# Kernel tuning notes

Hardware: AMD Instinct MI355X
Metric: run time of the kernel (lower is better)

## Reference

```python
import jax, jax.numpy as jnp
import numpy as np

EMBED_DIM = 1024
HEAD_SIZE = 256
B, T = 8, 2048


def setup_inputs() -> dict:
    key = jax.random.key(0)
    kx, kq, kk, kv = jax.random.split(key, 4)
    x = jax.random.normal(kx, (B, T, EMBED_DIM), dtype=jnp.float32)
    # torch Linear(E, H, bias=False): weight [H, E], y = x @ W.T; store as [E, H]
    s = 1.0 / np.sqrt(EMBED_DIM)
    Wq = jax.random.uniform(kq, (EMBED_DIM, HEAD_SIZE), jnp.float32, -s, s)
    Wk = jax.random.uniform(kk, (EMBED_DIM, HEAD_SIZE), jnp.float32, -s, s)
    Wv = jax.random.uniform(kv, (EMBED_DIM, HEAD_SIZE), jnp.float32, -s, s)
    return {"x": x, "Wq": Wq, "Wk": Wk, "Wv": Wv}


def reference(x, Wq, Wk, Wv):
    # x: [B, T, E]
    q = jnp.einsum("bte,eh->bth", x, Wq)
    k = jnp.einsum("bte,eh->bth", x, Wk)
    v = jnp.einsum("bte,eh->bth", x, Wv)
    scale = HEAD_SIZE ** -0.5
    scores = jnp.einsum("bth,bsh->bts", q, k) * scale  # [B, T, T]
    t = x.shape[1]
    causal = jnp.tril(jnp.ones((t, t), dtype=bool))
    scores = jnp.where(causal, scores, -jnp.inf)
    attn = jax.nn.softmax(scores, axis=-1)  # dropout p=0.0 -> identity
    return jnp.einsum("bts,bsh->bth", attn, v)
```

## Files before the change

kernel.cpp:

```cpp
#include <hip/hip_runtime.h>
#include <stdint.h>

#define EMBED 1024
#define HEAD  256
#define BATCH 8
#define SEQ   2048
#define NTOK  (BATCH*SEQ)

typedef __attribute__((ext_vector_type(8)))  short  s16x8;
typedef __attribute__((ext_vector_type(4)))  float  f32x4;
typedef __attribute__((ext_vector_type(16))) float  f32x16;
typedef __attribute__((ext_vector_type(4)))  unsigned short u16x4;

__device__ __forceinline__ unsigned short f2bf(float f) {
  union { float f; uint32_t u; } v; v.f = f;
  return (unsigned short)((v.u + 0x7FFFu + ((v.u >> 16) & 1u)) >> 16);
}

__device__ __forceinline__ uint32_t cvtpk(float a, float b) {
  uint32_t r;
  asm("v_cvt_pk_bf16_f32 %0, %1, %2" : "=v"(r) : "v"(a), "v"(b));
  return r;
}

__device__ __forceinline__ void gload_lds16(const void* g, void* l) {
  __builtin_amdgcn_global_load_lds((const __attribute__((address_space(1))) void*)g,
                                   (__attribute__((address_space(3))) void*)l, 16, 0, 0);
}

__global__ __launch_bounds__(256) void wt_kernel(const float* __restrict__ Wq,
                                                 const float* __restrict__ Wk,
                                                 const float* __restrict__ Wv,
                                                 unsigned short* __restrict__ Wt) {
  int idx = blockIdx.x * 256 + threadIdx.x;
  int e  = idx & (EMBED - 1);
  int hw = idx >> 10;
  int w  = hw >> 8;
  int h  = hw & 255;
  const float* W = (w == 0) ? Wq : (w == 1) ? Wk : Wv;
  float sc = (w == 0) ? 0.0625f : 1.0f;
  Wt[idx] = f2bf(W[(size_t)e * HEAD + h] * sc);
}

__global__ __launch_bounds__(256) void xprep_kernel(const float* __restrict__ x,
                                                    unsigned short* __restrict__ xb) {
  size_t i8 = ((size_t)blockIdx.x * 256 + threadIdx.x) * 8;
  f32x4 f0 = *(const f32x4*)(x + i8);
  f32x4 f1 = *(const f32x4*)(x + i8 + 4);
  u16x4 p0, p1;
  #pragma unroll
  for (int j = 0; j < 4; j++) { p0[j] = f2bf(f0[j]); p1[j] = f2bf(f1[j]); }
  *(u16x4*)(xb + i8)     = p0;
  *(u16x4*)(xb + i8 + 4) = p1;
}

__global__ __launch_bounds__(256) void proj_kernel(const unsigned short* __restrict__ xb,
    const unsigned short* __restrict__ Wt,
    unsigned short* __restrict__ qo, unsigned short* __restrict__ ko,
    unsigned short* __restrict__ vfrag) {
  __shared__ unsigned short Al[128 * 64];
  __shared__ unsigned short Bl[128 * 64];
  const int tid  = threadIdx.x;
  const int lane = tid & 63;
  const int wid  = tid >> 6;
  const int wm = wid >> 1, wn = wid & 1;
  const int bid  = blockIdx.x;
  const int xcd  = bid & 7;
  const int i6   = bid >> 3;
  const int mloc = i6 & 15;
  const int nz   = i6 >> 4;
  const int m0 = (xcd * 16 + mloc) * 128;
  const int n0 = (nz & 1) * 128;
  const int w  = nz >> 1;
  const unsigned short* Wtw = Wt + (size_t)w * 256 * EMBED;

  f32x4 acc[4][4] = {};

  for (int k0 = 0; k0 < EMBED; k0 += 64) {
    #pragma unroll
    for (int i = 0; i < 4; i++) {
      int u = tid + 256 * i;
      int row = u >> 3, sc = u & 7;
      gload_lds16(xb + (size_t)(m0 + row) * EMBED + k0 + sc * 8,
                  &Al[i * 2048 + wid * 512]);
    }
    #pragma unroll
    for (int i = 0; i < 4; i++) {
      int u = tid + 256 * i;
      int row = u >> 3, sc = u & 7;
      gload_lds16(Wtw + (size_t)(n0 + row) * EMBED + k0 + sc * 8,
                  &Bl[i * 2048 + wid * 512]);
    }
    __syncthreads();
    #pragma unroll
    for (int kk = 0; kk < 2; kk++) {
      s16x8 a[4], bfr[4];
      #pragma unroll
      for (int mi = 0; mi < 4; mi++) {
        int row = wm * 64 + mi * 16 + (lane & 15);
        a[mi] = *(const s16x8*)(&Al[row * 64 + kk * 32 + 8 * (lane >> 4)]);
      }
      #pragma unroll
      for (int ni = 0; ni < 4; ni++) {
        int row = wn * 64 + ni * 16 + (lane & 15);
        bfr[ni] = *(const s16x8*)(&Bl[row * 64 + kk * 32 + 8 * (lane >> 4)]);
      }
      #pragma unroll
      for (int mi = 0; mi < 4; mi++)
        #pragma unroll
        for (int ni = 0; ni < 4; ni++)
          acc[mi][ni] = __builtin_amdgcn_mfma_f32_16x16x32_bf16(a[mi], bfr[ni], acc[mi][ni], 0, 0, 0);
    }
    __syncthreads();
  }

  if (w < 2) {
    unsigned short* dst = (w == 0) ? qo : ko;
    #pragma unroll
    for (int mi = 0; mi < 4; mi++)
      #pragma unroll
      for (int r = 0; r < 4; r++) {
        int mrow = m0 + wm * 64 + mi * 16 + 4 * (lane >> 4) + r;
        #pragma unroll
        for (int ni = 0; ni < 4; ni++) {
          int col = n0 + wn * 64 + ni * 16 + (lane & 15);
          dst[(size_t)mrow * HEAD + col] = f2bf(acc[mi][ni][r]);
        }
      }
  } else {
    #pragma unroll
    for (int mi = 0; mi < 4; mi++) {
      int base = m0 + wm * 64 + mi * 16 + 4 * (lane >> 4);
      int toko = base & 31;
      size_t vb0 = (size_t)(base >> 11) * 524288
                 + (size_t)((base & 2047) >> 5) * 8192
                 + ((toko >> 4) & 1) * 512 + ((toko >> 3) & 1) * 256 + (toko & 7);
      #pragma unroll
      for (int ni = 0; ni < 4; ni++) {
        int col = n0 + wn * 64 + ni * 16 + (lane & 15);
        u16x4 pk;
        #pragma unroll
        for (int r = 0; r < 4; r++) pk[r] = f2bf(acc[mi][ni][r]);
        *(u16x4*)(vfrag + vb0 + (size_t)(col >> 5) * 1024 + (col & 31) * 8) = pk;
      }
    }
  }
}

__global__ __launch_bounds__(256, 1) void attn_kernel(const unsigned short* __restrict__ qb,
    const unsigned short* __restrict__ kb, const unsigned short* __restrict__ vfrag,
    float* __restrict__ out) {
  __shared__ unsigned short Kl[4][32 * 256];
  __shared__ float mls[4][2][32];
  const int tid  = threadIdx.x;
  const int lane = tid & 63;
  const int w    = tid >> 6;
  const int hi   = lane >> 5;
  const int q    = lane & 31;
  const int bid  = blockIdx.x;
  const int b = bid & 7;
  const int p = bid >> 3;
  const unsigned short* qB = qb + (size_t)b * SEQ * HEAD;
  const unsigned short* kB = kb + (size_t)b * SEQ * HEAD;
  const unsigned short* vfB = vfrag + (size_t)b * 524288;
  float* outB = out + (size_t)b * SEQ * HEAD;
  unsigned short* Kw = (unsigned short*)Kl[w];

  for (int sl = 0; sl < 2; sl++) {
    const int t  = sl ? p : (63 - p);
    const int qg = t * 32 + q;

    s16x8 qf[16];
    #pragma unroll
    for (int s = 0; s < 16; s++)
      qf[s] = *(const s16x8*)(qB + (size_t)qg * HEAD + s * 16 + hi * 8);

    f32x16 o[8] = {};
    float m = -1e30f, lsum = 0.f;

    const int nt = t + 1;
    const int cl = (nt + 3) >> 2;
    const int j0 = w * cl;
    const int j1 = (j0 + cl < nt) ? (j0 + cl) : nt;

    for (int j = j0; j < j1; j++) {
      #pragma unroll
      for (int i = 0; i < 16; i++) {
        int cl_ = i * 64 + lane;
        int key = cl_ >> 5, c = cl_ & 31;
        gload_lds16(kB + (size_t)(j * 32 + key) * HEAD + (size_t)((c ^ (key & 15)) * 8),
                    &Kw[i * 512]);
      }
      asm volatile("s_waitcnt vmcnt(0)" ::: "memory");
      __builtin_amdgcn_sched_barrier(0);
      f32x16 s0 = {}, s1 = {};
      #pragma unroll
      for (int s = 0; s < 8; s++) {
        s16x8 kf = *(const s16x8*)((const char*)Kw +
                     (q * 512 + (((2 * s + hi) ^ (q & 15)) << 4)));
        s0 = __builtin_amdgcn_mfma_f32_32x32x16_bf16(kf, qf[s], s0, 0, 0, 0);
      }
      #pragma unroll
      for (int s = 8; s < 16; s++) {
        s16x8 kf = *(const s16x8*)((const char*)Kw +
                     (q * 512 + (((2 * s + hi) ^ (q & 15)) << 4)));
        s1 = __builtin_amdgcn_mfma_f32_32x32x16_bf16(kf, qf[s], s1, 0, 0, 0);
      }
      f32x16 sv;
      #pragma unroll
      for (int r = 0; r < 16; r++) sv[r] = s0[r] + s1[r];
      if (j == t) {
        #pragma unroll
        for (int r = 0; r < 16; r++) {
          int kg = j * 32 + (r & 3) + 8 * (r >> 2) + 4 * hi;
          sv[r] = (kg > qg) ? -1e30f : sv[r];
        }
      }
      float mt = sv[0];
      #pragma unroll
      for (int r = 1; r < 16; r++) mt = fmaxf(mt, sv[r]);
      mt = fmaxf(mt, __shfl_xor(mt, 32));
      float mn = fmaxf(m, mt);
      if (!__all(mt - m <= 8.0f)) {
        float al = __expf(m - mn);
        lsum *= al;
        #pragma unroll
        for (int ht = 0; ht < 8; ht++)
          #pragma unroll
          for (int r = 0; r < 16; r++) o[ht][r] *= al;
        m = mn;
      }
      #pragma unroll
      for (int r = 0; r < 16; r++) sv[r] = __expf(sv[r] - m);
      float rs = 0.f;
      #pragma unroll
      for (int r = 0; r < 16; r++) rs += sv[r];
      rs += __shfl_xor(rs, 32);
      lsum += rs;
      uint32_t cc[8], dd[8];
      #pragma unroll
      for (int i = 0; i < 8; i++) cc[i] = cvtpk(sv[2 * i], sv[2 * i + 1]);
      #pragma unroll
      for (int i = 0; i < 8; i++) dd[i] = (uint32_t)__shfl_xor((int)cc[i], 32);
      union { s16x8 v; uint32_t u[4]; } pf0, pf1;
      pf0.u[0] = hi ? dd[2] : cc[0];
      pf0.u[1] = hi ? dd[3] : cc[1];
      pf0.u[2] = hi ? cc[2] : dd[0];
      pf0.u[3] = hi ? cc[3] : dd[1];
      pf1.u[0] = hi ? dd[6] : cc[4];
      pf1.u[1] = hi ? dd[7] : cc[5];
      pf1.u[2] = hi ? cc[6] : dd[4];
      pf1.u[3] = hi ? cc[7] : dd[5];
      const unsigned short* vT = vfB + (size_t)j * 8192 + hi * 256 + q * 8;
      #pragma unroll
      for (int ht = 0; ht < 8; ht++) {
        s16x8 vf0 = *(const s16x8*)(vT + ht * 1024);
        o[ht] = __builtin_amdgcn_mfma_f32_32x32x16_bf16(vf0, pf0.v, o[ht], 0, 0, 0);
        s16x8 vf1 = *(const s16x8*)(vT + ht * 1024 + 512);
        o[ht] = __builtin_amdgcn_mfma_f32_32x32x16_bf16(vf1, pf1.v, o[ht], 0, 0, 0);
      }
    }

    __syncthreads();
    if (lane < 32) { mls[w][0][q] = m; mls[w][1][q] = lsum; }
    __syncthreads();
    float mx = mls[0][0][q];
    #pragma unroll
    for (int w2 = 1; w2 < 4; w2++) mx = fmaxf(mx, mls[w2][0][q]);
    float L = 0.f;
    #pragma unroll
    for (int w2 = 0; w2 < 4; w2++)
      L += __expf(mls[w2][0][q] - mx) * mls[w2][1][q];
    float aown = __expf(m - mx);
    #pragma unroll
    for (int ht = 0; ht < 8; ht++)
      #pragma unroll
      for (int r = 0; r < 16; r++) o[ht][r] *= aown;

    float* obuf = (float*)&Kl[0][0];
    for (int ph = 3; ph >= 0; ph--) {
      if (w == ph) {
        #pragma unroll
        for (int ht = 0; ht < 8; ht++)
          #pragma unroll
          for (int g2 = 0; g2 < 4; g2++) {
            int gp = 8 * ht + 2 * g2 + hi;
            float* ptr = &obuf[q * 256 + ((gp ^ (q & 15)) << 2)];
            f32x4 v4 = { o[ht][4*g2], o[ht][4*g2+1], o[ht][4*g2+2], o[ht][4*g2+3] };
            if (ph != 3) { f32x4 prev = *(f32x4*)ptr;
              #pragma unroll
              for (int z = 0; z < 4; z++) v4[z] += prev[z]; }
            if (ph != 0) { *(f32x4*)ptr = v4; }
            else {
              #pragma unroll
              for (int z = 0; z < 4; z++) v4[z] /= L;
              *(f32x4*)(outB + (size_t)qg * HEAD + ht * 32 + g2 * 8 + hi * 4) = v4;
            }
          }
      }
      __syncthreads();
    }
  }
}

extern "C" void kernel_launch(void* const* d_in, const int* in_sizes, int n_in,
                              void* d_out, int out_size, void* d_ws, size_t ws_size,
                              hipStream_t stream) {
  const float* x  = (const float*)d_in[0];
  const float* Wq = (const float*)d_in[1];
  const float* Wk = (const float*)d_in[2];
  const float* Wv = (const float*)d_in[3];
  float* out = (float*)d_out;

  unsigned short* ws = (unsigned short*)d_ws;
  unsigned short* qb    = ws;
  unsigned short* kb    = qb + (size_t)NTOK * HEAD;
  unsigned short* vfrag = kb + (size_t)NTOK * HEAD;
  unsigned short* Wt    = vfrag + (size_t)NTOK * HEAD;
  unsigned short* xb    = Wt + (size_t)3 * HEAD * EMBED;

  hipLaunchKernelGGL(wt_kernel, dim3(3 * 256 * EMBED / 256), dim3(256), 0, stream,
                     Wq, Wk, Wv, Wt);
  hipLaunchKernelGGL(xprep_kernel, dim3(NTOK * EMBED / (256 * 8)), dim3(256), 0, stream,
                     x, xb);
  hipLaunchKernelGGL(proj_kernel, dim3(768), dim3(256), 0, stream,
                     xb, Wt, qb, kb, vfrag);
  hipLaunchKernelGGL(attn_kernel, dim3(256), dim3(256), 0, stream,
                     qb, kb, vfrag, out);
}
```

Baseline: 144.6 us.

## Split attention KV range across two blocks with merge kernel, use exp2

Each query tile's causal key range is split into two halves handled by separate blocks, doubling the grid to 512 blocks. Each block writes bf16 partial outputs plus per-row max and sum to workspace, and a new merge kernel combines the two halves and normalizes. The Q scale now folds in log2(e) so softmax can use exp2f instead of __expf, with the rescale threshold adjusted to match. This adds an extra launch, extra workspace traffic, and bf16 rounding of the partial outputs.

```diff
diff --git a/kernel.cpp b/kernel.cpp
--- a/kernel.cpp
+++ b/kernel.cpp
@@ -15,6 +15,10 @@
 __device__ __forceinline__ unsigned short f2bf(float f) {
   union { float f; uint32_t u; } v; v.f = f;
   return (unsigned short)((v.u + 0x7FFFu + ((v.u >> 16) & 1u)) >> 16);
+}
+
+__device__ __forceinline__ float b2f(unsigned short u) {
+  union { uint32_t u; float f; } v; v.u = (uint32_t)u << 16; return v.f;
 }
 
 __device__ __forceinline__ uint32_t cvtpk(float a, float b) {
@@ -38,7 +42,7 @@
   int w  = hw >> 8;
   int h  = hw & 255;
   const float* W = (w == 0) ? Wq : (w == 1) ? Wk : Wv;
-  float sc = (w == 0) ? 0.0625f : 1.0f;
+  float sc = (w == 0) ? 0.09016844f : 1.0f;
   Wt[idx] = f2bf(W[(size_t)e * HEAD + h] * sc);
 }
 
@@ -149,7 +153,7 @@
 
 __global__ __launch_bounds__(256, 1) void attn_kernel(const unsigned short* __restrict__ qb,
     const unsigned short* __restrict__ kb, const unsigned short* __restrict__ vfrag,
-    float* __restrict__ out) {
+    unsigned short* __restrict__ po, float* __restrict__ pml) {
   __shared__ unsigned short Kl[4][32 * 256];
   __shared__ float mls[4][2][32];
   const int tid  = threadIdx.x;
@@ -158,12 +162,13 @@
   const int hi   = lane >> 5;
   const int q    = lane & 31;
   const int bid  = blockIdx.x;
-  const int b = bid & 7;
-  const int p = bid >> 3;
+  const int b  = bid & 7;
+  const int r2 = bid >> 3;
+  const int p  = r2 >> 1;
+  const int h  = r2 & 1;
   const unsigned short* qB = qb + (size_t)b * SEQ * HEAD;
   const unsigned short* kB = kb + (size_t)b * SEQ * HEAD;
   const unsigned short* vfB = vfrag + (size_t)b * 524288;
-  float* outB = out + (size_t)b * SEQ * HEAD;
   unsigned short* Kw = (unsigned short*)Kl[w];
 
   for (int sl = 0; sl < 2; sl++) {
@@ -178,10 +183,14 @@
     f32x16 o[8] = {};
     float m = -1e30f, lsum = 0.f;
 
-    const int nt = t + 1;
-    const int cl = (nt + 3) >> 2;
-    const int j0 = w * cl;
-    const int j1 = (j0 + cl < nt) ? (j0 + cl) : nt;
+    const int nt  = t + 1;
+    const int hc0 = (nt + 1) >> 1;
+    const int st  = h ? hc0 : 0;
+    const int cnt = h ? (nt - hc0) : hc0;
+    const int cl  = (cnt + 3) >> 2;
+    const int j0  = st + w * cl;
+    const int j1e = st + cnt;
+    const int j1  = (j0 + cl < j1e) ? (j0 + cl) : j1e;
 
     for (int j = j0; j < j1; j++) {
       #pragma unroll
@@ -221,8 +230,8 @@
       for (int r = 1; r < 16; r++) mt = fmaxf(mt, sv[r]);
       mt = fmaxf(mt, __shfl_xor(mt, 32));
       float mn = fmaxf(m, mt);
-      if (!__all(mt - m <= 8.0f)) {
-        float al = __expf(m - mn);
+      if (!__all(mt - m <= 11.5416f)) {
+        float al = exp2f(m - mn);
         lsum *= al;
         #pragma unroll
         for (int ht = 0; ht < 8; ht++)
@@ -231,7 +240,7 @@
         m = mn;
       }
       #pragma unroll
-      for (int r = 0; r < 16; r++) sv[r] = __expf(sv[r] - m);
+      for (int r = 0; r < 16; r++) sv[r] = exp2f(sv[r] - m);
       float rs = 0.f;
       #pragma unroll
       for (int r = 0; r < 16; r++) rs += sv[r];
@@ -270,12 +279,19 @@
     float L = 0.f;
     #pragma unroll
     for (int w2 = 0; w2 < 4; w2++)
-      L += __expf(mls[w2][0][q] - mx) * mls[w2][1][q];
-    float aown = __expf(m - mx);
+      L += exp2f(mls[w2][0][q] - mx) * mls[w2][1][q];
+    float aown = exp2f(m - mx);
     #pragma unroll
     for (int ht = 0; ht < 8; ht++)
       #pragma unroll
       for (int r = 0; r < 16; r++) o[ht][r] *= aown;
+
+    const int pid = (b * 64 + t) * 2 + h;
+    unsigned short* poS = po + (size_t)pid * 8192;
+    if (w == 0 && lane < 32) {
+      pml[pid * 64 + lane] = mx;
+      pml[pid * 64 + 32 + lane] = L;
+    }
 
     float* obuf = (float*)&Kl[0][0];
     for (int ph = 3; ph >= 0; ph--) {
@@ -292,14 +308,46 @@
               for (int z = 0; z < 4; z++) v4[z] += prev[z]; }
             if (ph != 0) { *(f32x4*)ptr = v4; }
             else {
+              u16x4 pk;
               #pragma unroll
-              for (int z = 0; z < 4; z++) v4[z] /= L;
-              *(f32x4*)(outB + (size_t)qg * HEAD + ht * 32 + g2 * 8 + hi * 4) = v4;
+              for (int z = 0; z < 4; z++) pk[z] = f2bf(v4[z]);
+              *(u16x4*)(poS + q * 256 + ht * 32 + g2 * 8 + hi * 4) = pk;
             }
           }
       }
       __syncthreads();
     }
+  }
+}
+
+__global__ __launch_bounds__(256) void fmerge_kernel(const unsigned short* __restrict__ po,
+    const float* __restrict__ pml, float* __restrict__ out) {
+  const int blk = blockIdx.x;
+  const int b = blk >> 6, t = blk & 63;
+  const int tid = threadIdx.x;
+  const int q = tid >> 3;
+  const int c0 = (tid & 7) * 32;
+  const int pid0 = (b * 64 + t) * 2;
+  float m0 = pml[pid0 * 64 + q],       L0 = pml[pid0 * 64 + 32 + q];
+  float m1 = pml[(pid0 + 1) * 64 + q], L1 = pml[(pid0 + 1) * 64 + 32 + q];
+  float M = fmaxf(m0, m1);
+  float a0 = exp2f(m0 - M), a1 = exp2f(m1 - M);
+  float L = a0 * L0 + a1 * L1;
+  const unsigned short* p0 = po + (size_t)pid0 * 8192 + q * 256 + c0;
+  const unsigned short* p1 = p0 + 8192;
+  float* op = out + ((size_t)b * SEQ + t * 32 + q) * HEAD + c0;
+  #pragma unroll
+  for (int i = 0; i < 4; i++) {
+    s16x8 x0 = *(const s16x8*)(p0 + i * 8);
+    s16x8 x1 = *(const s16x8*)(p1 + i * 8);
+    f32x4 lo, hi2;
+    #pragma unroll
+    for (int z = 0; z < 4; z++) {
+      lo[z]  = (a0 * b2f((unsigned short)x0[z])     + a1 * b2f((unsigned short)x1[z]))     / L;
+      hi2[z] = (a0 * b2f((unsigned short)x0[z + 4]) + a1 * b2f((unsigned short)x1[z + 4])) / L;
+    }
+    *(f32x4*)(op + i * 8)     = lo;
+    *(f32x4*)(op + i * 8 + 4) = hi2;
   }
 }
 
@@ -318,6 +366,8 @@
   unsigned short* vfrag = kb + (size_t)NTOK * HEAD;
   unsigned short* Wt    = vfrag + (size_t)NTOK * HEAD;
   unsigned short* xb    = Wt + (size_t)3 * HEAD * EMBED;
+  unsigned short* po    = xb;
+  float*          pml   = (float*)(xb + (size_t)1024 * 8192);
 
   hipLaunchKernelGGL(wt_kernel, dim3(3 * 256 * EMBED / 256), dim3(256), 0, stream,
                      Wq, Wk, Wv, Wt);
@@ -325,6 +375,8 @@
                      x, xb);
   hipLaunchKernelGGL(proj_kernel, dim3(768), dim3(256), 0, stream,
                      xb, Wt, qb, kb, vfrag);
-  hipLaunchKernelGGL(attn_kernel, dim3(256), dim3(256), 0, stream,
-                     qb, kb, vfrag, out);
-}
+  hipLaunchKernelGGL(attn_kernel, dim3(512), dim3(256), 0, stream,
+                     qb, kb, vfrag, po, pml);
+  hipLaunchKernelGGL(fmerge_kernel, dim3(512), dim3(256), 0, stream,
+                     po, pml, out);
+}
```

Result: slower. 165.8 us (+14.7%).
